# Optimization experiments

Measured on AMD Instinct MI355X. Metric: run time of the kernel, lower is better.

Reference implementation:

```python
import jax, jax.numpy as jnp
import numpy as np

N_NODES = 100000
FEAT_DIM = 256
EMBED_DIM = 256
BATCH = 50000
NUM_SAMPLE = 25
NAN_FILL = 0.01  # neigh_feats[isnan] = 0.01 in the original


def setup_inputs() -> dict:
    key = jax.random.key(0)
    k1, k2, k3, k4 = jax.random.split(key, 4)
    features = jax.random.normal(k1, (N_NODES, FEAT_DIM), dtype=jnp.float32)
    # Xavier-uniform-ish weight [embed_dim, feat_dim + embed_dim] (gcn=True)
    fan = FEAT_DIM + EMBED_DIM
    bound = float(np.sqrt(6.0 / (EMBED_DIM + fan)))
    weight = jax.random.uniform(k2, (EMBED_DIM, fan), dtype=jnp.float32,
                                minval=-bound, maxval=bound)
    nodes = jax.random.randint(k3, (BATCH,), 0, N_NODES, dtype=jnp.int64)
    neigh_idx = jax.random.randint(k4, (BATCH, NUM_SAMPLE), 0, N_NODES, dtype=jnp.int64)
    return {"features": features, "weight": weight, "nodes": nodes,
            "neigh_idx": neigh_idx}


def reference(features, weight, nodes, neigh_idx):
    # MeanAggregator: gather sampled neighbor features and mean over neighbors
    neigh_feats = features[neigh_idx].mean(axis=1)            # [B, F]
    neigh_feats = jnp.where(jnp.isnan(neigh_feats), NAN_FILL, neigh_feats)
    self_feats = features[nodes]                              # [B, F]
    combined = jnp.concatenate([self_feats, neigh_feats], axis=1)  # [B, F+E]
    # weight.matmul(combined.t()) then ReLU -> [E, B]
    out = jax.nn.relu(jnp.einsum('ef,bf->eb', weight, combined))
    return out
```

## Files before the change

### kernel.cpp

```cpp
#include <hip/hip_runtime.h>
#include <hip/hip_bf16.h>

#define FEAT    256
#define KDIM    512
#define EMBED   256
#define BATCH   50000
#define NSAMP   25
#define N_NODES 100000
#define NAN_FILL 0.01f

#define NTILE   48
#define LSTRIDE 520

#define FCONV_BLOCKS 12500
#define WCONV_BLOCKS 64

typedef __attribute__((ext_vector_type(8))) short  short8;
typedef __attribute__((ext_vector_type(4))) float  floatx4;
typedef __attribute__((ext_vector_type(2))) float  float2v;
typedef __attribute__((ext_vector_type(4))) unsigned short ushort4v;
typedef __attribute__((ext_vector_type(4))) float  float4v;

__device__ inline unsigned short f2bf(float x) {
    __hip_bfloat16 h = __float2bfloat16(x);
    union { __hip_bfloat16 h; unsigned short u; } c; c.h = h;
    return c.u;
}

__global__ __launch_bounds__(256) void conv_kernel(
    const float* __restrict__ F, unsigned char* __restrict__ F8,
    unsigned short* __restrict__ Fb,
    const float* __restrict__ W, unsigned short* __restrict__ Wb)
{
    if (blockIdx.x < FCONV_BLOCKS) {
        const size_t i = ((size_t)blockIdx.x * 256 + threadIdx.x) * 8;
        float4v a = *(const float4v*)(F + i);
        float4v b = *(const float4v*)(F + i + 4);
        int p0 = 0, p1 = 0;
        p0 = __builtin_amdgcn_cvt_pk_fp8_f32(a[0], a[1], p0, false);
        p0 = __builtin_amdgcn_cvt_pk_fp8_f32(a[2], a[3], p0, true);
        p1 = __builtin_amdgcn_cvt_pk_fp8_f32(b[0], b[1], p1, false);
        p1 = __builtin_amdgcn_cvt_pk_fp8_f32(b[2], b[3], p1, true);
        uint2 o; o.x = (unsigned)p0; o.y = (unsigned)p1;
        *(uint2*)(F8 + i) = o;
        ushort4v o0, o1;
        o0[0] = f2bf(a[0]); o0[1] = f2bf(a[1]); o0[2] = f2bf(a[2]); o0[3] = f2bf(a[3]);
        o1[0] = f2bf(b[0]); o1[1] = f2bf(b[1]); o1[2] = f2bf(b[2]); o1[3] = f2bf(b[3]);
        *(ushort4v*)(Fb + i) = o0;
        *(ushort4v*)(Fb + i + 4) = o1;
    } else {
        const size_t i = ((size_t)(blockIdx.x - FCONV_BLOCKS) * 256 + threadIdx.x) * 8;
        float4v a = *(const float4v*)(W + i);
        float4v b = *(const float4v*)(W + i + 4);
        ushort4v o0, o1;
        o0[0] = f2bf(a[0]); o0[1] = f2bf(a[1]); o0[2] = f2bf(a[2]); o0[3] = f2bf(a[3]);
        o1[0] = f2bf(b[0]); o1[1] = f2bf(b[1]); o1[2] = f2bf(b[2]); o1[3] = f2bf(b[3]);
        *(ushort4v*)(Wb + i) = o0;
        *(ushort4v*)(Wb + i + 4) = o1;
    }
}

__global__ __launch_bounds__(256, 3) void enc_kernel(
    const unsigned char* __restrict__ F8,
    const unsigned short* __restrict__ Fb,
    const unsigned short* __restrict__ Wb,
    const int* __restrict__ nodes,
    const int* __restrict__ neigh,
    float* __restrict__ out)
{
    __shared__ unsigned short cl[NTILE * LSTRIDE];

    const int lane = threadIdx.x & 63;
    const int wave = threadIdx.x >> 6;
    const int q = lane >> 4;
    const int r = lane & 15;
    const int nbase = blockIdx.x * NTILE;

    for (int it = 0; it < NTILE / 4; ++it) {
        const int li = wave * (NTILE / 4) + it;
        int b = nbase + li;
        if (b >= BATCH) b = BATCH - 1;

        const int node = nodes[b];
        ushort4v sv = *(const ushort4v*)(Fb + (size_t)node * FEAT + lane * 4);

        const int* nb = neigh + (size_t)b * NSAMP;
        float s0 = 0.f, s1 = 0.f, s2 = 0.f, s3 = 0.f;
        #pragma unroll
        for (int j = 0; j < NSAMP; ++j) {
            const int idx = nb[j];
            int wv = *(const int*)(F8 + (size_t)idx * FEAT + lane * 4);
            float2v lo = __builtin_amdgcn_cvt_pk_f32_fp8(wv, false);
            float2v hi = __builtin_amdgcn_cvt_pk_f32_fp8(wv, true);
            s0 += lo[0]; s1 += lo[1]; s2 += hi[0]; s3 += hi[1];
        }
        const float inv = 1.0f / NSAMP;
        float m0 = s0 * inv, m1 = s1 * inv, m2 = s2 * inv, m3 = s3 * inv;
        if (m0 != m0) m0 = NAN_FILL;
        if (m1 != m1) m1 = NAN_FILL;
        if (m2 != m2) m2 = NAN_FILL;
        if (m3 != m3) m3 = NAN_FILL;

        unsigned short* row = cl + li * LSTRIDE;
        *(ushort4v*)(row + lane * 4) = sv;
        ushort4v m; m[0] = f2bf(m0); m[1] = f2bf(m1); m[2] = f2bf(m2); m[3] = f2bf(m3);
        *(ushort4v*)(row + FEAT + lane * 4) = m;
    }
    __syncthreads();

    const int mbase = wave * 64;
    const short* Wp = (const short*)Wb;
    const short* cp = (const short*)cl;

    floatx4 acc[4][3] = {};

    for (int k = 0; k < KDIM; k += 32) {
        short8 afr[4], bfr[3];
        #pragma unroll
        for (int mt = 0; mt < 4; ++mt) {
            const short* p = Wp + (size_t)(mbase + mt * 16 + r) * KDIM + k + q * 8;
            afr[mt] = *(const short8*)p;
        }
        #pragma unroll
        for (int nt = 0; nt < 3; ++nt) {
            const short* p = cp + (nt * 16 + r) * LSTRIDE + k + q * 8;
            bfr[nt] = *(const short8*)p;
        }
        #pragma unroll
        for (int mt = 0; mt < 4; ++mt)
            #pragma unroll
            for (int nt = 0; nt < 3; ++nt)
                acc[mt][nt] = __builtin_amdgcn_mfma_f32_16x16x32_bf16(
                    afr[mt], bfr[nt], acc[mt][nt], 0, 0, 0);
    }

    #pragma unroll
    for (int mt = 0; mt < 4; ++mt) {
        #pragma unroll
        for (int nt = 0; nt < 3; ++nt) {
            const int col = nbase + nt * 16 + r;
            if (col < BATCH) {
                #pragma unroll
                for (int i = 0; i < 4; ++i) {
                    const int row = mbase + mt * 16 + q * 4 + i;
                    float v = acc[mt][nt][i];
                    out[(size_t)row * BATCH + col] = v > 0.f ? v : 0.f;
                }
            }
        }
    }
}

extern "C" void kernel_launch(void* const* d_in, const int* in_sizes, int n_in,
                              void* d_out, int out_size, void* d_ws, size_t ws_size,
                              hipStream_t stream) {
    const float* features = (const float*)d_in[0];
    const float* weight   = (const float*)d_in[1];
    const int*   nodes    = (const int*)d_in[2];
    const int*   neigh    = (const int*)d_in[3];
    float* out = (float*)d_out;

    unsigned char*  F8 = (unsigned char*)d_ws;
    unsigned short* Wb = (unsigned short*)(F8 + (size_t)N_NODES * FEAT);
    unsigned short* Fb = Wb + (size_t)EMBED * KDIM;

    conv_kernel<<<FCONV_BLOCKS + WCONV_BLOCKS, 256, 0, stream>>>(
        features, F8, Fb, weight, Wb);

    const int nblocks = (BATCH + NTILE - 1) / NTILE;
    enc_kernel<<<nblocks, 256, 0, stream>>>(F8, Fb, Wb, nodes, neigh, out);
}
```

Baseline: 267.6 us.

## Stage neighbor indices in LDS, XOR-swizzle combined tile, unroll gather loop

At block start, all neighbor indices and node ids for the tile are loaded cooperatively into shared memory. This replaces the scalar per-row global index loads sitting on the gather's dependency chain. The padded LDS row stride is replaced by an XOR swizzle on 16-byte chunks to avoid bank conflicts for both the writes and the MFMA B-fragment reads. The gather loop is also unrolled by 2 to expose more memory-level parallelism, at the cost of extra LDS, an added barrier and more register pressure.

```diff
diff --git a/kernel.cpp b/kernel.cpp
--- a/kernel.cpp
+++ b/kernel.cpp
@@ -10,7 +10,6 @@
 #define NAN_FILL 0.01f
 
 #define NTILE   48
-#define LSTRIDE 520
 
 #define FCONV_BLOCKS 12500
 #define WCONV_BLOCKS 64
@@ -68,7 +67,9 @@
     const int* __restrict__ neigh,
     float* __restrict__ out)
 {
-    __shared__ unsigned short cl[NTILE * LSTRIDE];
+    __shared__ unsigned short cl[NTILE * 512];
+    __shared__ int idxbuf[NTILE * NSAMP];
+    __shared__ int nodebuf[NTILE];
 
     const int lane = threadIdx.x & 63;
     const int wave = threadIdx.x >> 6;
@@ -76,19 +77,38 @@
     const int r = lane & 15;
     const int nbase = blockIdx.x * NTILE;
 
+    {
+        const size_t gbase = (size_t)nbase * NSAMP;
+        const size_t gmax  = (size_t)BATCH * NSAMP - 1;
+        #pragma unroll
+        for (int t = 0; t < 5; ++t) {
+            const int p = t * 256 + threadIdx.x;
+            if (p < NTILE * NSAMP) {
+                size_t g = gbase + p;
+                if (g > gmax) g = gmax;
+                idxbuf[p] = neigh[g];
+            }
+        }
+        if (threadIdx.x < NTILE) {
+            int bb = nbase + threadIdx.x;
+            if (bb >= BATCH) bb = BATCH - 1;
+            nodebuf[threadIdx.x] = nodes[bb];
+        }
+    }
+    __syncthreads();
+
+    #pragma unroll 2
     for (int it = 0; it < NTILE / 4; ++it) {
         const int li = wave * (NTILE / 4) + it;
-        int b = nbase + li;
-        if (b >= BATCH) b = BATCH - 1;
+        const int sw = li & 7;
 
-        const int node = nodes[b];
+        const int node = nodebuf[li];
         ushort4v sv = *(const ushort4v*)(Fb + (size_t)node * FEAT + lane * 4);
 
-        const int* nb = neigh + (size_t)b * NSAMP;
         float s0 = 0.f, s1 = 0.f, s2 = 0.f, s3 = 0.f;
         #pragma unroll
         for (int j = 0; j < NSAMP; ++j) {
-            const int idx = nb[j];
+            const int idx = idxbuf[li * NSAMP + j];
             int wv = *(const int*)(F8 + (size_t)idx * FEAT + lane * 4);
             float2v lo = __builtin_amdgcn_cvt_pk_f32_fp8(wv, false);
             float2v hi = __builtin_amdgcn_cvt_pk_f32_fp8(wv, true);
@@ -101,10 +121,10 @@
         if (m2 != m2) m2 = NAN_FILL;
         if (m3 != m3) m3 = NAN_FILL;
 
-        unsigned short* row = cl + li * LSTRIDE;
-        *(ushort4v*)(row + lane * 4) = sv;
+        unsigned short* rowp = cl + li * 512;
+        *(ushort4v*)(rowp + ((((lane >> 1) ^ sw) << 3) | ((lane & 1) << 2))) = sv;
         ushort4v m; m[0] = f2bf(m0); m[1] = f2bf(m1); m[2] = f2bf(m2); m[3] = f2bf(m3);
-        *(ushort4v*)(row + FEAT + lane * 4) = m;
+        *(ushort4v*)(rowp + ((((32 + (lane >> 1)) ^ sw) << 3) | ((lane & 1) << 2))) = m;
     }
     __syncthreads();
 
@@ -123,7 +143,8 @@
         }
         #pragma unroll
         for (int nt = 0; nt < 3; ++nt) {
-            const short* p = cp + (nt * 16 + r) * LSTRIDE + k + q * 8;
+            const int li = nt * 16 + r;
+            const short* p = cp + (size_t)li * 512 + ((((k >> 3) + q) ^ (r & 7)) << 3);
             bfr[nt] = *(const short8*)p;
         }
         #pragma unroll
```

Measured after the change: 275.5 us. 1.03x slower.

## Double block to 512 threads and split neighbor gather across half-waves

Applied to the files above, without the earlier changes.

The encoder block grows from 4 to 8 waves. Each wave now handles 6 batch rows instead of 12 and computes 32 output rows of the MFMA tile instead of 64. In the neighbor gather, each half-wave loads a different neighbor with 8-byte fp8 loads, and the two halves' sums are combined with a cross-lane shuffle. This halves the serial gather chain per row and doubles memory-level parallelism, at the cost of more register pressure from 8 accumulators and the extra shuffles. The weight operand is reloaded by more waves, and the launch bound asks for 6 blocks per CU.

```diff
diff --git a/kernel.cpp b/kernel.cpp
--- a/kernel.cpp
+++ b/kernel.cpp
@@ -19,6 +19,7 @@
 typedef __attribute__((ext_vector_type(4))) float  floatx4;
 typedef __attribute__((ext_vector_type(2))) float  float2v;
 typedef __attribute__((ext_vector_type(4))) unsigned short ushort4v;
+typedef __attribute__((ext_vector_type(8))) unsigned short ushort8v;
 typedef __attribute__((ext_vector_type(4))) float  float4v;
 
 __device__ inline unsigned short f2bf(float x) {
@@ -60,7 +61,7 @@
     }
 }
 
-__global__ __launch_bounds__(256, 3) void enc_kernel(
+__global__ __launch_bounds__(512, 6) void enc_kernel(
     const unsigned char* __restrict__ F8,
     const unsigned short* __restrict__ Fb,
     const unsigned short* __restrict__ Wb,
@@ -74,10 +75,12 @@
     const int wave = threadIdx.x >> 6;
     const int q = lane >> 4;
     const int r = lane & 15;
+    const int half = lane >> 5;
+    const int hl = lane & 31;
     const int nbase = blockIdx.x * NTILE;
 
-    for (int it = 0; it < NTILE / 4; ++it) {
-        const int li = wave * (NTILE / 4) + it;
+    for (int it = 0; it < NTILE / 8; ++it) {
+        const int li = wave * (NTILE / 8) + it;
         int b = nbase + li;
         if (b >= BATCH) b = BATCH - 1;
 
@@ -85,39 +88,63 @@
         ushort4v sv = *(const ushort4v*)(Fb + (size_t)node * FEAT + lane * 4);
 
         const int* nb = neigh + (size_t)b * NSAMP;
-        float s0 = 0.f, s1 = 0.f, s2 = 0.f, s3 = 0.f;
+        float s0=0.f,s1=0.f,s2=0.f,s3=0.f,s4=0.f,s5=0.f,s6=0.f,s7=0.f;
+
         #pragma unroll
-        for (int j = 0; j < NSAMP; ++j) {
-            const int idx = nb[j];
-            int wv = *(const int*)(F8 + (size_t)idx * FEAT + lane * 4);
-            float2v lo = __builtin_amdgcn_cvt_pk_f32_fp8(wv, false);
-            float2v hi = __builtin_amdgcn_cvt_pk_f32_fp8(wv, true);
-            s0 += lo[0]; s1 += lo[1]; s2 += hi[0]; s3 += hi[1];
+        for (int j = 0; j < NSAMP - 1; j += 2) {
+            const int iA = nb[j];
+            const int iB = nb[j + 1];
+            const int idx = half ? iB : iA;
+            uint2 wv = *(const uint2*)(F8 + (size_t)idx * FEAT + hl * 8);
+            float2v a0 = __builtin_amdgcn_cvt_pk_f32_fp8((int)wv.x, false);
+            float2v a1 = __builtin_amdgcn_cvt_pk_f32_fp8((int)wv.x, true);
+            float2v a2 = __builtin_amdgcn_cvt_pk_f32_fp8((int)wv.y, false);
+            float2v a3 = __builtin_amdgcn_cvt_pk_f32_fp8((int)wv.y, true);
+            s0 += a0[0]; s1 += a0[1]; s2 += a1[0]; s3 += a1[1];
+            s4 += a2[0]; s5 += a2[1]; s6 += a3[0]; s7 += a3[1];
         }
+        {
+            const int iL = nb[NSAMP - 1];
+            uint2 wv = *(const uint2*)(F8 + (size_t)iL * FEAT + hl * 8);
+            if (half) { wv.x = 0u; wv.y = 0u; }
+            float2v a0 = __builtin_amdgcn_cvt_pk_f32_fp8((int)wv.x, false);
+            float2v a1 = __builtin_amdgcn_cvt_pk_f32_fp8((int)wv.x, true);
+            float2v a2 = __builtin_amdgcn_cvt_pk_f32_fp8((int)wv.y, false);
+            float2v a3 = __builtin_amdgcn_cvt_pk_f32_fp8((int)wv.y, true);
+            s0 += a0[0]; s1 += a0[1]; s2 += a1[0]; s3 += a1[1];
+            s4 += a2[0]; s5 += a2[1]; s6 += a3[0]; s7 += a3[1];
+        }
+        s0 += __shfl_xor(s0, 32, 64); s1 += __shfl_xor(s1, 32, 64);
+        s2 += __shfl_xor(s2, 32, 64); s3 += __shfl_xor(s3, 32, 64);
+        s4 += __shfl_xor(s4, 32, 64); s5 += __shfl_xor(s5, 32, 64);
+        s6 += __shfl_xor(s6, 32, 64); s7 += __shfl_xor(s7, 32, 64);
+
         const float inv = 1.0f / NSAMP;
-        float m0 = s0 * inv, m1 = s1 * inv, m2 = s2 * inv, m3 = s3 * inv;
-        if (m0 != m0) m0 = NAN_FILL;
-        if (m1 != m1) m1 = NAN_FILL;
-        if (m2 != m2) m2 = NAN_FILL;
-        if (m3 != m3) m3 = NAN_FILL;
+        float m[8] = { s0*inv, s1*inv, s2*inv, s3*inv, s4*inv, s5*inv, s6*inv, s7*inv };
+        #pragma unroll
+        for (int e = 0; e < 8; ++e) if (m[e] != m[e]) m[e] = NAN_FILL;
 
-        unsigned short* row = cl + li * LSTRIDE;
-        *(ushort4v*)(row + lane * 4) = sv;
-        ushort4v m; m[0] = f2bf(m0); m[1] = f2bf(m1); m[2] = f2bf(m2); m[3] = f2bf(m3);
-        *(ushort4v*)(row + FEAT + lane * 4) = m;
+        unsigned short* rowp = cl + li * LSTRIDE;
+        *(ushort4v*)(rowp + lane * 4) = sv;
+        if (half == 0) {
+            ushort8v mv;
+            #pragma unroll
+            for (int e = 0; e < 8; ++e) mv[e] = f2bf(m[e]);
+            *(ushort8v*)(rowp + FEAT + hl * 8) = mv;
+        }
     }
     __syncthreads();
 
-    const int mbase = wave * 64;
+    const int mbase = wave * 32;
     const short* Wp = (const short*)Wb;
     const short* cp = (const short*)cl;
 
-    floatx4 acc[4][3] = {};
+    floatx4 acc[2][3] = {};
 
     for (int k = 0; k < KDIM; k += 32) {
-        short8 afr[4], bfr[3];
+        short8 afr[2], bfr[3];
         #pragma unroll
-        for (int mt = 0; mt < 4; ++mt) {
+        for (int mt = 0; mt < 2; ++mt) {
             const short* p = Wp + (size_t)(mbase + mt * 16 + r) * KDIM + k + q * 8;
             afr[mt] = *(const short8*)p;
         }
@@ -127,7 +154,7 @@
             bfr[nt] = *(const short8*)p;
         }
         #pragma unroll
-        for (int mt = 0; mt < 4; ++mt)
+        for (int mt = 0; mt < 2; ++mt)
             #pragma unroll
             for (int nt = 0; nt < 3; ++nt)
                 acc[mt][nt] = __builtin_amdgcn_mfma_f32_16x16x32_bf16(
@@ -135,7 +162,7 @@
     }
 
     #pragma unroll
-    for (int mt = 0; mt < 4; ++mt) {
+    for (int mt = 0; mt < 2; ++mt) {
         #pragma unroll
         for (int nt = 0; nt < 3; ++nt) {
             const int col = nbase + nt * 16 + r;
@@ -168,5 +195,5 @@
         features, F8, Fb, weight, Wb);
 
     const int nblocks = (BATCH + NTILE - 1) / NTILE;
-    enc_kernel<<<nblocks, 256, 0, stream>>>(F8, Fb, Wb, nodes, neigh, out);
+    enc_kernel<<<nblocks, 512, 0, stream>>>(F8, Fb, Wb, nodes, neigh, out);
 }
```

Result: no change. 270.3 us (+1.0%).
